# Kernel tuning notes

Measured on AMD Instinct MI355X. Metric: run time of the kernel, lower is better.

## Reference

```python
import jax, jax.numpy as jnp
import numpy as np

# (multiplicity, irrep dimension 2l+1) for '64x0e + 32x1o + 16x2e' (in == out)
SEGMENTS = [(64, 1), (32, 3), (16, 5)]
N = 200000
IN_DIM = sum(u * i for u, i in SEGMENTS)          # 240
W_NUMEL = sum(u * u for u, _ in SEGMENTS)          # 5376


def setup_inputs() -> dict:
    key = jax.random.key(0)
    kx, kw = jax.random.split(key)
    x = jax.random.normal(kx, (N, IN_DIM), dtype=jnp.float32)
    weight = jax.random.normal(kw, (1, W_NUMEL), dtype=jnp.float32)
    return {"x": x, "weight": weight}


def reference(x, weight):
    """Equivariant linear: per-irrep 'uv,iu,iv' channel mixing (mul_ir layout)."""
    w = weight[0]
    n = x.shape[0]
    outs = []
    xo = 0
    wo = 0
    for u, i in SEGMENTS:
        v = u  # irreps_out == irreps_in
        xs = x[:, xo:xo + u * i].reshape(n, u, i)      # [N, u, i]
        ws = w[wo:wo + u * v].reshape(u, v)            # [u, v]
        # path normalization 1/sqrt(u_in)
        o = jnp.einsum('nui,uv->nvi', xs, ws) * (1.0 / np.sqrt(u))
        outs.append(o.reshape(n, v * i))
        xo += u * i
        wo += u * v
    return jnp.concatenate(outs, axis=1)               # [N, 240]
```

## Files before the change

### kernel.cpp

```cpp
#include <hip/hip_runtime.h>


#define TILE 32
#define BLOCK 256

__global__ __launch_bounds__(BLOCK, 3) void eqlin_kernel(
    const float* __restrict__ x, const float* __restrict__ w,
    float* __restrict__ out, int nrows)
{
    __shared__ __align__(16) float xs[TILE * 240];
    __shared__ __align__(16) float ws[5376];

    const int tid = threadIdx.x;
    const long long row0 = (long long)blockIdx.x * TILE;

    {
        const float4* wg = (const float4*)w;
        float4* wl = (float4*)ws;
        #pragma unroll 2
        for (int idx = tid; idx < 1344; idx += BLOCK) wl[idx] = wg[idx];
    }
    {
        const float4* xg = (const float4*)(x + row0 * 240);
        float4* xl = (float4*)xs;
        #pragma unroll 2
        for (int idx = tid; idx < 1920; idx += BLOCK) xl[idx] = xg[idx];
    }
    __syncthreads();

    const int lane = tid & 63;
    const int wvid = tid >> 6;
    const int rb = wvid * 8;

    {
        const int v = lane;
        float acc[8];
        #pragma unroll
        for (int r = 0; r < 8; ++r) acc[r] = 0.f;
        #pragma unroll 4
        for (int k = 0; k < 16; ++k) {
            const float w0 = ws[(4*k+0)*64 + v];
            const float w1 = ws[(4*k+1)*64 + v];
            const float w2 = ws[(4*k+2)*64 + v];
            const float w3 = ws[(4*k+3)*64 + v];
            #pragma unroll
            for (int r = 0; r < 8; ++r) {
                const float4 xq = *(const float4*)&xs[(rb + r)*240 + 4*k];
                acc[r] += xq.x*w0 + xq.y*w1 + xq.z*w2 + xq.w*w3;
            }
        }
        #pragma unroll
        for (int r = 0; r < 8; ++r) xs[(rb + r)*240 + v] = acc[r] * 0.125f;
    }

    {
        const int v  = lane & 31;
        const int h  = lane >> 5;
        const int r0 = rb + h * 4;
        float acc[4][3];
        #pragma unroll
        for (int r = 0; r < 4; ++r)
            #pragma unroll
            for (int i = 0; i < 3; ++i) acc[r][i] = 0.f;
        #pragma unroll 4
        for (int k = 0; k < 8; ++k) {
            const float w0 = ws[4096 + (4*k+0)*32 + v];
            const float w1 = ws[4096 + (4*k+1)*32 + v];
            const float w2 = ws[4096 + (4*k+2)*32 + v];
            const float w3 = ws[4096 + (4*k+3)*32 + v];
            #pragma unroll
            for (int r = 0; r < 4; ++r) {
                const float* xr = &xs[(r0 + r)*240 + 64 + 12*k];
                const float4 a = *(const float4*)(xr);
                const float4 b = *(const float4*)(xr + 4);
                const float4 c = *(const float4*)(xr + 8);
                acc[r][0] += a.x*w0 + a.w*w1 + b.z*w2 + c.y*w3;
                acc[r][1] += a.y*w0 + b.x*w1 + b.w*w2 + c.z*w3;
                acc[r][2] += a.z*w0 + b.y*w1 + c.x*w2 + c.w*w3;
            }
        }
        const float s1 = 0.17677669529663687f;
        #pragma unroll
        for (int r = 0; r < 4; ++r)
            #pragma unroll
            for (int i = 0; i < 3; ++i)
                xs[(r0 + r)*240 + 64 + v*3 + i] = acc[r][i] * s1;
    }

    {
        const int v  = lane & 15;
        const int q  = lane >> 4;
        const int r0 = rb + q * 2;
        float acc[2][5];
        #pragma unroll
        for (int r = 0; r < 2; ++r)
            #pragma unroll
            for (int i = 0; i < 5; ++i) acc[r][i] = 0.f;
        #pragma unroll
        for (int k = 0; k < 4; ++k) {
            const float w0 = ws[5120 + (4*k+0)*16 + v];
            const float w1 = ws[5120 + (4*k+1)*16 + v];
            const float w2 = ws[5120 + (4*k+2)*16 + v];
            const float w3 = ws[5120 + (4*k+3)*16 + v];
            #pragma unroll
            for (int r = 0; r < 2; ++r) {
                const float* xr = &xs[(r0 + r)*240 + 160 + 20*k];
                const float4 a = *(const float4*)(xr);
                const float4 b = *(const float4*)(xr + 4);
                const float4 c = *(const float4*)(xr + 8);
                const float4 d = *(const float4*)(xr + 12);
                const float4 e = *(const float4*)(xr + 16);
                acc[r][0] += a.x*w0 + b.y*w1 + c.z*w2 + d.w*w3;
                acc[r][1] += a.y*w0 + b.z*w1 + c.w*w2 + e.x*w3;
                acc[r][2] += a.z*w0 + b.w*w1 + d.x*w2 + e.y*w3;
                acc[r][3] += a.w*w0 + c.x*w1 + d.y*w2 + e.z*w3;
                acc[r][4] += b.x*w0 + c.y*w1 + d.z*w2 + e.w*w3;
            }
        }
        #pragma unroll
        for (int r = 0; r < 2; ++r)
            #pragma unroll
            for (int i = 0; i < 5; ++i)
                xs[(r0 + r)*240 + 160 + v*5 + i] = acc[r][i] * 0.25f;
    }

    __syncthreads();

    {
        float4* og = (float4*)(out + row0 * 240);
        const float4* xl = (const float4*)xs;
        #pragma unroll 2
        for (int idx = tid; idx < 1920; idx += BLOCK) og[idx] = xl[idx];
    }
}

extern "C" void kernel_launch(void* const* d_in, const int* in_sizes, int n_in,
                              void* d_out, int out_size, void* d_ws, size_t ws_size,
                              hipStream_t stream) {
    const float* x = (const float*)d_in[0];
    const float* w = (const float*)d_in[1];
    float* out = (float*)d_out;
    const int nrows = in_sizes[0] / 240;
    const int blocks = nrows / TILE;
    eqlin_kernel<<<blocks, BLOCK, 0, stream>>>(x, w, out, nrows);
}
```

Measured before the change: 352.4 us.

## Read weights directly from global/L2 and make each wave own its rows

```diff
diff --git a/kernel.cpp b/kernel.cpp
--- a/kernel.cpp
+++ b/kernel.cpp
@@ -4,33 +4,26 @@
 #define TILE 32
 #define BLOCK 256
 
-__global__ __launch_bounds__(BLOCK, 3) void eqlin_kernel(
+__global__ __launch_bounds__(BLOCK, 5) void eqlin_kernel(
     const float* __restrict__ x, const float* __restrict__ w,
     float* __restrict__ out, int nrows)
 {
     __shared__ __align__(16) float xs[TILE * 240];
-    __shared__ __align__(16) float ws[5376];
 
-    const int tid = threadIdx.x;
+    const int tid  = threadIdx.x;
+    const int lane = tid & 63;
+    const int wvid = tid >> 6;
+    const int rb   = wvid * 8;
     const long long row0 = (long long)blockIdx.x * TILE;
 
     {
-        const float4* wg = (const float4*)w;
-        float4* wl = (float4*)ws;
-        #pragma unroll 2
-        for (int idx = tid; idx < 1344; idx += BLOCK) wl[idx] = wg[idx];
+        const float4* __restrict__ xg = (const float4*)(x + (row0 + rb) * 240);
+        float4* xl = (float4*)(xs + rb * 240);
+        #pragma unroll
+        for (int j = 0; j < 7; ++j) xl[j * 64 + lane] = xg[j * 64 + lane];
+        if (lane < 32) xl[448 + lane] = xg[448 + lane];
     }
-    {
-        const float4* xg = (const float4*)(x + row0 * 240);
-        float4* xl = (float4*)xs;
-        #pragma unroll 2
-        for (int idx = tid; idx < 1920; idx += BLOCK) xl[idx] = xg[idx];
-    }
-    __syncthreads();
-
-    const int lane = tid & 63;
-    const int wvid = tid >> 6;
-    const int rb = wvid * 8;
+    __builtin_amdgcn_wave_barrier();
 
     {
         const int v = lane;
@@ -39,10 +32,10 @@
         for (int r = 0; r < 8; ++r) acc[r] = 0.f;
         #pragma unroll 4
         for (int k = 0; k < 16; ++k) {
-            const float w0 = ws[(4*k+0)*64 + v];
-            const float w1 = ws[(4*k+1)*64 + v];
-            const float w2 = ws[(4*k+2)*64 + v];
-            const float w3 = ws[(4*k+3)*64 + v];
+            const float w0 = w[(4*k+0)*64 + v];
+            const float w1 = w[(4*k+1)*64 + v];
+            const float w2 = w[(4*k+2)*64 + v];
+            const float w3 = w[(4*k+3)*64 + v];
             #pragma unroll
             for (int r = 0; r < 8; ++r) {
                 const float4 xq = *(const float4*)&xs[(rb + r)*240 + 4*k];
@@ -57,6 +50,7 @@
         const int v  = lane & 31;
         const int h  = lane >> 5;
         const int r0 = rb + h * 4;
+        const float* __restrict__ w1p = w + 4096;
         float acc[4][3];
         #pragma unroll
         for (int r = 0; r < 4; ++r)
@@ -64,10 +58,10 @@
             for (int i = 0; i < 3; ++i) acc[r][i] = 0.f;
         #pragma unroll 4
         for (int k = 0; k < 8; ++k) {
-            const float w0 = ws[4096 + (4*k+0)*32 + v];
-            const float w1 = ws[4096 + (4*k+1)*32 + v];
-            const float w2 = ws[4096 + (4*k+2)*32 + v];
-            const float w3 = ws[4096 + (4*k+3)*32 + v];
+            const float w0 = w1p[(4*k+0)*32 + v];
+            const float w1 = w1p[(4*k+1)*32 + v];
+            const float w2 = w1p[(4*k+2)*32 + v];
+            const float w3 = w1p[(4*k+3)*32 + v];
             #pragma unroll
             for (int r = 0; r < 4; ++r) {
                 const float* xr = &xs[(r0 + r)*240 + 64 + 12*k];
@@ -91,6 +85,7 @@
         const int v  = lane & 15;
         const int q  = lane >> 4;
         const int r0 = rb + q * 2;
+        const float* __restrict__ w2p = w + 5120;
         float acc[2][5];
         #pragma unroll
         for (int r = 0; r < 2; ++r)
@@ -98,10 +93,10 @@
             for (int i = 0; i < 5; ++i) acc[r][i] = 0.f;
         #pragma unroll
         for (int k = 0; k < 4; ++k) {
-            const float w0 = ws[5120 + (4*k+0)*16 + v];
-            const float w1 = ws[5120 + (4*k+1)*16 + v];
-            const float w2 = ws[5120 + (4*k+2)*16 + v];
-            const float w3 = ws[5120 + (4*k+3)*16 + v];
+            const float w0 = w2p[(4*k+0)*16 + v];
+            const float w1 = w2p[(4*k+1)*16 + v];
+            const float w2 = w2p[(4*k+2)*16 + v];
+            const float w3 = w2p[(4*k+3)*16 + v];
             #pragma unroll
             for (int r = 0; r < 2; ++r) {
                 const float* xr = &xs[(r0 + r)*240 + 160 + 20*k];
@@ -124,13 +119,14 @@
                 xs[(r0 + r)*240 + 160 + v*5 + i] = acc[r][i] * 0.25f;
     }
 
-    __syncthreads();
+    __builtin_amdgcn_wave_barrier();
 
     {
-        float4* og = (float4*)(out + row0 * 240);
-        const float4* xl = (const float4*)xs;
-        #pragma unroll 2
-        for (int idx = tid; idx < 1920; idx += BLOCK) og[idx] = xl[idx];
+        float4* og = (float4*)(out + (row0 + rb) * 240);
+        const float4* xl = (const float4*)(xs + rb * 240);
+        #pragma unroll
+        for (int j = 0; j < 7; ++j) og[j * 64 + lane] = xl[j * 64 + lane];
+        if (lane < 32) og[448 + lane] = xl[448 + lane];
     }
 }
 
```

After: 364.5 us. 3.4% more time.

## Drop shared-memory x staging; read rows directly from global with register tiling

Applied to the files above, without the earlier changes.

```diff
diff --git a/kernel.cpp b/kernel.cpp
--- a/kernel.cpp
+++ b/kernel.cpp
@@ -1,136 +1,144 @@
 #include <hip/hip_runtime.h>
 
 
-#define TILE 32
 #define BLOCK 256
+#define RPB 64
+#define RPW 16
 
-__global__ __launch_bounds__(BLOCK, 3) void eqlin_kernel(
+#define FMA4(acc, q, w0, w1, w2, w3)                         \
+    acc.x += q.x*w0.x + q.y*w1.x + q.z*w2.x + q.w*w3.x;      \
+    acc.y += q.x*w0.y + q.y*w1.y + q.z*w2.y + q.w*w3.y;      \
+    acc.z += q.x*w0.z + q.y*w1.z + q.z*w2.z + q.w*w3.z;      \
+    acc.w += q.x*w0.w + q.y*w1.w + q.z*w2.w + q.w*w3.w;
+
+__global__ __launch_bounds__(BLOCK, 5) void eqlin_kernel(
     const float* __restrict__ x, const float* __restrict__ w,
     float* __restrict__ out, int nrows)
 {
-    __shared__ __align__(16) float xs[TILE * 240];
     __shared__ __align__(16) float ws[5376];
 
     const int tid = threadIdx.x;
-    const long long row0 = (long long)blockIdx.x * TILE;
-
     {
         const float4* wg = (const float4*)w;
         float4* wl = (float4*)ws;
         #pragma unroll 2
         for (int idx = tid; idx < 1344; idx += BLOCK) wl[idx] = wg[idx];
     }
-    {
-        const float4* xg = (const float4*)(x + row0 * 240);
-        float4* xl = (float4*)xs;
-        #pragma unroll 2
-        for (int idx = tid; idx < 1920; idx += BLOCK) xl[idx] = xg[idx];
-    }
     __syncthreads();
 
     const int lane = tid & 63;
     const int wvid = tid >> 6;
-    const int rb = wvid * 8;
+    const int rowbase = blockIdx.x * RPB + wvid * RPW;
+    if (rowbase >= nrows) return;
 
     {
-        const int v = lane;
-        float acc[8];
-        #pragma unroll
-        for (int r = 0; r < 8; ++r) acc[r] = 0.f;
+        const int vg = lane & 15;
+        const int rg = lane >> 4;
+        const float* xr0 = x + (rowbase + rg * 4) * 240;
+        float4 acc0 = {0,0,0,0}, acc1 = {0,0,0,0}, acc2 = {0,0,0,0}, acc3 = {0,0,0,0};
         #pragma unroll 4
-        for (int k = 0; k < 16; ++k) {
-            const float w0 = ws[(4*k+0)*64 + v];
-            const float w1 = ws[(4*k+1)*64 + v];
-            const float w2 = ws[(4*k+2)*64 + v];
-            const float w3 = ws[(4*k+3)*64 + v];
-            #pragma unroll
-            for (int r = 0; r < 8; ++r) {
-                const float4 xq = *(const float4*)&xs[(rb + r)*240 + 4*k];
-                acc[r] += xq.x*w0 + xq.y*w1 + xq.z*w2 + xq.w*w3;
-            }
+        for (int kg = 0; kg < 16; ++kg) {
+            const float4 w0 = *(const float4*)&ws[(4*kg + 0) * 64 + 4*vg];
+            const float4 w1 = *(const float4*)&ws[(4*kg + 1) * 64 + 4*vg];
+            const float4 w2 = *(const float4*)&ws[(4*kg + 2) * 64 + 4*vg];
+            const float4 w3 = *(const float4*)&ws[(4*kg + 3) * 64 + 4*vg];
+            const float4 q0 = *(const float4*)(xr0 +   0 + 4*kg);
+            const float4 q1 = *(const float4*)(xr0 + 240 + 4*kg);
+            const float4 q2 = *(const float4*)(xr0 + 480 + 4*kg);
+            const float4 q3 = *(const float4*)(xr0 + 720 + 4*kg);
+            FMA4(acc0, q0, w0, w1, w2, w3);
+            FMA4(acc1, q1, w0, w1, w2, w3);
+            FMA4(acc2, q2, w0, w1, w2, w3);
+            FMA4(acc3, q3, w0, w1, w2, w3);
         }
-        #pragma unroll
-        for (int r = 0; r < 8; ++r) xs[(rb + r)*240 + v] = acc[r] * 0.125f;
+        float* ob = out + (rowbase + rg * 4) * 240 + 4*vg;
+        const float4 s = {0.125f, 0.125f, 0.125f, 0.125f};
+        float4 o;
+        o.x = acc0.x*s.x; o.y = acc0.y*s.x; o.z = acc0.z*s.x; o.w = acc0.w*s.x;
+        *(float4*)(ob +   0) = o;
+        o.x = acc1.x*s.x; o.y = acc1.y*s.x; o.z = acc1.z*s.x; o.w = acc1.w*s.x;
+        *(float4*)(ob + 240) = o;
+        o.x = acc2.x*s.x; o.y = acc2.y*s.x; o.z = acc2.z*s.x; o.w = acc2.w*s.x;
+        *(float4*)(ob + 480) = o;
+        o.x = acc3.x*s.x; o.y = acc3.y*s.x; o.z = acc3.z*s.x; o.w = acc3.w*s.x;
+        *(float4*)(ob + 720) = o;
     }
 
     {
-        const int v  = lane & 31;
-        const int h  = lane >> 5;
-        const int r0 = rb + h * 4;
-        float acc[4][3];
-        #pragma unroll
-        for (int r = 0; r < 4; ++r)
-            #pragma unroll
-            for (int i = 0; i < 3; ++i) acc[r][i] = 0.f;
-        #pragma unroll 4
-        for (int k = 0; k < 8; ++k) {
-            const float w0 = ws[4096 + (4*k+0)*32 + v];
-            const float w1 = ws[4096 + (4*k+1)*32 + v];
-            const float w2 = ws[4096 + (4*k+2)*32 + v];
-            const float w3 = ws[4096 + (4*k+3)*32 + v];
+        const int vg = lane & 15;
+        const int rg = lane >> 4;
+        const float* xb = x + (rowbase + rg * 4) * 240 + 64;
+        float acc[4][6] = {};
+        #pragma unroll 2
+        for (int kg = 0; kg < 8; ++kg) {
+            const float2 p0 = *(const float2*)&ws[4096 + (4*kg + 0) * 32 + 2*vg];
+            const float2 p1 = *(const float2*)&ws[4096 + (4*kg + 1) * 32 + 2*vg];
+            const float2 p2 = *(const float2*)&ws[4096 + (4*kg + 2) * 32 + 2*vg];
+            const float2 p3 = *(const float2*)&ws[4096 + (4*kg + 3) * 32 + 2*vg];
             #pragma unroll
             for (int r = 0; r < 4; ++r) {
-                const float* xr = &xs[(r0 + r)*240 + 64 + 12*k];
+                const float* xr = xb + r * 240 + 12*kg;
                 const float4 a = *(const float4*)(xr);
                 const float4 b = *(const float4*)(xr + 4);
                 const float4 c = *(const float4*)(xr + 8);
-                acc[r][0] += a.x*w0 + a.w*w1 + b.z*w2 + c.y*w3;
-                acc[r][1] += a.y*w0 + b.x*w1 + b.w*w2 + c.z*w3;
-                acc[r][2] += a.z*w0 + b.y*w1 + c.x*w2 + c.w*w3;
+                acc[r][0] += a.x*p0.x + a.w*p1.x + b.z*p2.x + c.y*p3.x;
+                acc[r][1] += a.y*p0.x + b.x*p1.x + b.w*p2.x + c.z*p3.x;
+                acc[r][2] += a.z*p0.x + b.y*p1.x + c.x*p2.x + c.w*p3.x;
+                acc[r][3] += a.x*p0.y + a.w*p1.y + b.z*p2.y + c.y*p3.y;
+                acc[r][4] += a.y*p0.y + b.x*p1.y + b.w*p2.y + c.z*p3.y;
+                acc[r][5] += a.z*p0.y + b.y*p1.y + c.x*p2.y + c.w*p3.y;
             }
         }
         const float s1 = 0.17677669529663687f;
         #pragma unroll
-        for (int r = 0; r < 4; ++r)
-            #pragma unroll
-            for (int i = 0; i < 3; ++i)
-                xs[(r0 + r)*240 + 64 + v*3 + i] = acc[r][i] * s1;
+        for (int r = 0; r < 4; ++r) {
+            float* op = out + (rowbase + rg * 4 + r) * 240 + 64 + 6*vg;
+            *(float2*)(op + 0) = make_float2(acc[r][0]*s1, acc[r][1]*s1);
+            *(float2*)(op + 2) = make_float2(acc[r][2]*s1, acc[r][3]*s1);
+            *(float2*)(op + 4) = make_float2(acc[r][4]*s1, acc[r][5]*s1);
+        }
     }
 
     {
-        const int v  = lane & 15;
-        const int q  = lane >> 4;
-        const int r0 = rb + q * 2;
-        float acc[2][5];
+        const int vg = lane & 7;
+        const int rg = lane >> 3;
+        const float* xb = x + (rowbase + rg * 2) * 240 + 160;
+        float acc[2][10] = {};
         #pragma unroll
-        for (int r = 0; r < 2; ++r)
-            #pragma unroll
-            for (int i = 0; i < 5; ++i) acc[r][i] = 0.f;
-        #pragma unroll
-        for (int k = 0; k < 4; ++k) {
-            const float w0 = ws[5120 + (4*k+0)*16 + v];
-            const float w1 = ws[5120 + (4*k+1)*16 + v];
-            const float w2 = ws[5120 + (4*k+2)*16 + v];
-            const float w3 = ws[5120 + (4*k+3)*16 + v];
+        for (int kg = 0; kg < 4; ++kg) {
+            const float2 p0 = *(const float2*)&ws[5120 + (4*kg + 0) * 16 + 2*vg];
+            const float2 p1 = *(const float2*)&ws[5120 + (4*kg + 1) * 16 + 2*vg];
+            const float2 p2 = *(const float2*)&ws[5120 + (4*kg + 2) * 16 + 2*vg];
+            const float2 p3 = *(const float2*)&ws[5120 + (4*kg + 3) * 16 + 2*vg];
             #pragma unroll
             for (int r = 0; r < 2; ++r) {
-                const float* xr = &xs[(r0 + r)*240 + 160 + 20*k];
+                const float* xr = xb + r * 240 + 20*kg;
                 const float4 a = *(const float4*)(xr);
                 const float4 b = *(const float4*)(xr + 4);
                 const float4 c = *(const float4*)(xr + 8);
                 const float4 d = *(const float4*)(xr + 12);
                 const float4 e = *(const float4*)(xr + 16);
-                acc[r][0] += a.x*w0 + b.y*w1 + c.z*w2 + d.w*w3;
-                acc[r][1] += a.y*w0 + b.z*w1 + c.w*w2 + e.x*w3;
-                acc[r][2] += a.z*w0 + b.w*w1 + d.x*w2 + e.y*w3;
-                acc[r][3] += a.w*w0 + c.x*w1 + d.y*w2 + e.z*w3;
-                acc[r][4] += b.x*w0 + c.y*w1 + d.z*w2 + e.w*w3;
+                acc[r][0] += a.x*p0.x + b.y*p1.x + c.z*p2.x + d.w*p3.x;
+                acc[r][1] += a.y*p0.x + b.z*p1.x + c.w*p2.x + e.x*p3.x;
+                acc[r][2] += a.z*p0.x + b.w*p1.x + d.x*p2.x + e.y*p3.x;
+                acc[r][3] += a.w*p0.x + c.x*p1.x + d.y*p2.x + e.z*p3.x;
+                acc[r][4] += b.x*p0.x + c.y*p1.x + d.z*p2.x + e.w*p3.x;
+                acc[r][5] += a.x*p0.y + b.y*p1.y + c.z*p2.y + d.w*p3.y;
+                acc[r][6] += a.y*p0.y + b.z*p1.y + c.w*p2.y + e.x*p3.y;
+                acc[r][7] += a.z*p0.y + b.w*p1.y + d.x*p2.y + e.y*p3.y;
+                acc[r][8] += a.w*p0.y + c.x*p1.y + d.y*p2.y + e.z*p3.y;
+                acc[r][9] += b.x*p0.y + c.y*p1.y + d.z*p2.y + e.w*p3.y;
             }
         }
         #pragma unroll
-        for (int r = 0; r < 2; ++r)
-            #pragma unroll
-            for (int i = 0; i < 5; ++i)
-                xs[(r0 + r)*240 + 160 + v*5 + i] = acc[r][i] * 0.25f;
-    }
-
-    __syncthreads();
-
-    {
-        float4* og = (float4*)(out + row0 * 240);
-        const float4* xl = (const float4*)xs;
-        #pragma unroll 2
-        for (int idx = tid; idx < 1920; idx += BLOCK) og[idx] = xl[idx];
+        for (int r = 0; r < 2; ++r) {
+            float* op = out + (rowbase + rg * 2 + r) * 240 + 160 + 10*vg;
+            *(float2*)(op + 0) = make_float2(acc[r][0]*0.25f, acc[r][1]*0.25f);
+            *(float2*)(op + 2) = make_float2(acc[r][2]*0.25f, acc[r][3]*0.25f);
+            *(float2*)(op + 4) = make_float2(acc[r][4]*0.25f, acc[r][5]*0.25f);
+            *(float2*)(op + 6) = make_float2(acc[r][6]*0.25f, acc[r][7]*0.25f);
+            *(float2*)(op + 8) = make_float2(acc[r][8]*0.25f, acc[r][9]*0.25f);
+        }
     }
 }
 
@@ -141,6 +149,6 @@
     const float* w = (const float*)d_in[1];
     float* out = (float*)d_out;
     const int nrows = in_sizes[0] / 240;
-    const int blocks = nrows / TILE;
+    const int blocks = nrows / RPB;
     eqlin_kernel<<<blocks, BLOCK, 0, stream>>>(x, w, out, nrows);
 }
```

After: 883.1 us. 2.51x slower.
